# Performance work log

Hardware: AMD Instinct MI355X
Metric: run time of the kernel (lower is better)

The kernel has to match this reference:

```python
import jax, jax.numpy as jnp
import numpy as np

PARENTS = [-1, 0, 0, 0, 1, 2, 3, 4, 5, 6, 7, 8, 9, 9, 9, 12, 13, 14, 16, 17, 18, 19, 20, 21]
K = 24          # num_joints (SMPL kinematic tree)
BONE = 12       # 3x3 rotation (9) + 3 rel offset
FEAT = 64       # local_feature_size
B = 65536       # batch
NIN = BONE + 1 + FEAT  # 77: bone_transform(13) concat parent feature(64)


def setup_inputs() -> dict:
    key = jax.random.key(0)
    ks = jax.random.split(key, 6)
    pose = jax.random.normal(ks[0], (B, K, 3, 3), jnp.float32)
    rel_joints = jax.random.normal(ks[1], (B, K, 3), jnp.float32)
    # proj_bone_prior: Linear(K*BONE -> FEAT)
    Wp = jax.random.normal(ks[2], (K * BONE, FEAT), jnp.float32) * 0.05
    bp = jnp.zeros((FEAT,), jnp.float32)
    # per-joint BoneMLP: Linear(NIN->NIN), ReLU, Linear(NIN->FEAT), ReLU (stacked over K)
    W1 = jax.random.normal(ks[3], (K, NIN, NIN), jnp.float32) * 0.05
    b1 = jnp.zeros((K, NIN), jnp.float32)
    W2 = jax.random.normal(ks[4], (K, NIN, FEAT), jnp.float32) * 0.05
    b2 = jnp.zeros((K, FEAT), jnp.float32)
    return {"pose": pose, "rel_joints": rel_joints, "Wp": Wp, "bp": bp,
            "W1": W1, "b1": b1, "W2": W2, "b2": b2}


def reference(pose, rel_joints, Wp, bp, W1, b1, W2, b2):
    Bn, Kn = rel_joints.shape[0], rel_joints.shape[1]
    bone_lengths = jnp.linalg.norm(rel_joints, axis=-1, keepdims=True)          # B,K,1
    bone_features = jnp.concatenate([pose.reshape(Bn, Kn, 9), rel_joints], -1)  # B,K,12
    root_bone_prior = bone_features.reshape(Bn, -1) @ Wp + bp                   # B,FEAT
    bone_transforms = jnp.concatenate([bone_features, bone_lengths], -1)        # B,K,13
    feats = [None] * Kn
    for i in range(Kn):  # fixed structural loop over kinematic tree (K=24)
        parent = PARENTS[i]
        pf = root_bone_prior if parent == -1 else feats[parent]
        x = jnp.concatenate([bone_transforms[:, i, :], pf], axis=-1)  # B,77
        h = jax.nn.relu(x @ W1[i] + b1[i])
        feats[i] = jax.nn.relu(h @ W2[i] + b2[i])
    return jnp.concatenate(feats, axis=-1)  # B, K*FEAT
```

## Files before the change

### kernel.cpp

```cpp
#include <hip/hip_runtime.h>
#include <hip/hip_bf16.h>
#include <math.h>

typedef __attribute__((ext_vector_type(8))) short short8;
typedef __attribute__((ext_vector_type(4))) short s4;
typedef __attribute__((ext_vector_type(4))) float f32x4;

#define NJ 24

#define F1_J   7680
#define F2_OFF (NJ*F1_J)
#define F2_J   6144
#define FP_OFF (F2_OFF + NJ*F2_J)
#define IMG_SHORTS (FP_OFF + 36*512)

#define MFMA(A,B,C) __builtin_amdgcn_mfma_f32_16x16x32_bf16((A),(B),(C),0,0,0)

__constant__ int ORD[24] = {0,1,4,7,10, 2,5,8,11, 3,6,9, 12,15, 13,16,18,20,22, 14,17,19,21,23};
__constant__ int PSL[24] = {1,0,1,1,1,  0,1,1,1,  0,0,0,  0,1,   0,1,1,1,1,    0,0,0,0,0};
__constant__ int SSL[24] = {0,1,1,1,-1, 1,1,1,-1, 0,0,0,  1,-1,  1,1,1,1,-1,   0,0,0,0,-1};

__device__ __forceinline__ short f2bf(float f) {
  union { float f; unsigned u; } v; v.f = f;
  unsigned r = v.u + 0x7FFFu + ((v.u >> 16) & 1u);
  return (short)(r >> 16);
}
__device__ __forceinline__ short sbf(float f) {
  __hip_bfloat16 h = __float2bfloat16(f);
  return *reinterpret_cast<short*>(&h);
}
__device__ __forceinline__ short8 pk8(f32x4 lo, f32x4 hi) {
  union { short8 s; unsigned u[4]; } r;
  asm("v_cvt_pk_bf16_f32 %0, %1, %2" : "=v"(r.u[0]) : "v"(lo[0]), "v"(lo[1]));
  asm("v_cvt_pk_bf16_f32 %0, %1, %2" : "=v"(r.u[1]) : "v"(lo[2]), "v"(lo[3]));
  asm("v_cvt_pk_bf16_f32 %0, %1, %2" : "=v"(r.u[2]) : "v"(hi[0]), "v"(hi[1]));
  asm("v_cvt_pk_bf16_f32 %0, %1, %2" : "=v"(r.u[3]) : "v"(hi[2]), "v"(hi[3]));
  return r.s;
}
__device__ __forceinline__ s4 pk4(f32x4 v) {
  union { s4 s; unsigned u[2]; } r;
  asm("v_cvt_pk_bf16_f32 %0, %1, %2" : "=v"(r.u[0]) : "v"(v[0]), "v"(v[1]));
  asm("v_cvt_pk_bf16_f32 %0, %1, %2" : "=v"(r.u[1]) : "v"(v[2]), "v"(v[3]));
  return r.s;
}
__device__ __forceinline__ f32x4 relu4(f32x4 v) {
  f32x4 r; r[0]=fmaxf(v[0],0.f); r[1]=fmaxf(v[1],0.f);
  r[2]=fmaxf(v[2],0.f); r[3]=fmaxf(v[3],0.f); return r;
}

__global__ __launch_bounds__(256) void prep_kernel(
    const float* __restrict__ W1, const float* __restrict__ W2,
    const float* __restrict__ Wp, const float* __restrict__ b1,
    const float* __restrict__ b2, short* __restrict__ img) {
  int t = blockIdx.x * 256 + threadIdx.x;
  if (t >= IMG_SHORTS) return;
  float v = 0.f;
  if (t < F2_OFF) {
    int i = t / F1_J, r = t % F1_J;
    int blk = r >> 9, q = r & 511;
    int ln = q >> 3, e = q & 7;
    int nt = blk / 3, s = blk - nt*3;
    int n  = nt*16 + (ln & 15);
    int kp = s*32 + (ln >> 4)*8 + e;
    if (kp == 13) {
      v = (n < 77) ? b1[i*77 + n] : (n == 77 ? 1.f : 0.f);
    } else if (n < 77) {
      if (kp < 13)                  v = W1[i*5929 + kp*77 + n];
      else if (kp >= 16 && kp < 80) v = W1[i*5929 + (kp-3)*77 + n];
    }
  } else if (t < FP_OFF) {
    int u = t - F2_OFF;
    int i = u / F2_J, r = u % F2_J;
    int blk = r >> 9, q = r & 511;
    int ln = q >> 3, e = q & 7;
    int nt = blk / 3, s = blk - nt*3;
    int n  = nt*16 + (ln & 15);
    int k  = s*32 + (ln >> 4)*8 + e;
    if (k < 77)       v = W2[i*4928 + k*64 + n];
    else if (k == 77) v = b2[i*64 + n];
  } else {
    int u = t - FP_OFF;
    int blk = u >> 9, q = u & 511;
    int ln = q >> 3, e = q & 7;
    int nt = blk / 9, s = blk - nt*9;
    int n  = nt*16 + (ln & 15);
    int kp = s*32 + (ln >> 4)*8 + e;
    int j, w;
    if (kp < 216) { j = kp / 9;       w = kp % 9; }
    else          { j = (kp-216) / 3; w = 9 + (kp-216) % 3; }
    v = Wp[(j*12 + w)*64 + n];
  }
  img[t] = f2bf(v);
}

#define ISSUE_W1(JN) do { \
  unsigned long long _b = img_u + (unsigned long long)(JN)*15360ull; \
  asm volatile( \
    "global_load_dwordx4 %0, %15, %16\n"  "global_load_dwordx4 %1, %15, %16 offset:1024\n" \
    "global_load_dwordx4 %2, %15, %16 offset:2048\n" "global_load_dwordx4 %3, %15, %16 offset:3072\n" \
    "global_load_dwordx4 %4, %15, %17\n"  "global_load_dwordx4 %5, %15, %17 offset:1024\n" \
    "global_load_dwordx4 %6, %15, %17 offset:2048\n" "global_load_dwordx4 %7, %15, %17 offset:3072\n" \
    "global_load_dwordx4 %8, %15, %18\n"  "global_load_dwordx4 %9, %15, %18 offset:1024\n" \
    "global_load_dwordx4 %10, %15, %18 offset:2048\n" "global_load_dwordx4 %11, %15, %18 offset:3072\n" \
    "global_load_dwordx4 %12, %15, %19\n" "global_load_dwordx4 %13, %15, %19 offset:1024\n" \
    "global_load_dwordx4 %14, %15, %19 offset:2048\n" \
    : "=&v"(fw1[0]),"=&v"(fw1[1]),"=&v"(fw1[2]),"=&v"(fw1[3]),"=&v"(fw1[4]), \
      "=&v"(fw1[5]),"=&v"(fw1[6]),"=&v"(fw1[7]),"=&v"(fw1[8]),"=&v"(fw1[9]), \
      "=&v"(fw1[10]),"=&v"(fw1[11]),"=&v"(fw1[12]),"=&v"(fw1[13]),"=&v"(fw1[14]) \
    : "v"(voff), "s"(_b), "s"(_b+4096ull), "s"(_b+8192ull), "s"(_b+12288ull) \
    : "memory"); \
} while(0)

#define ISSUE_BTW2(J) do { \
  unsigned long long _b = img_u + 368640ull + (unsigned long long)(J)*12288ull; \
  asm volatile( \
    "global_load_dwordx4 %12, %26, %27\n" "global_load_dwordx4 %13, %26, %27 offset:1024\n" \
    "global_load_dwordx4 %14, %26, %27 offset:2048\n" "global_load_dwordx4 %15, %26, %27 offset:3072\n" \
    "global_load_dwordx4 %16, %26, %28\n" "global_load_dwordx4 %17, %26, %28 offset:1024\n" \
    "global_load_dwordx4 %18, %26, %28 offset:2048\n" "global_load_dwordx4 %19, %26, %28 offset:3072\n" \
    "global_load_dwordx4 %20, %26, %29\n" "global_load_dwordx4 %21, %26, %29 offset:1024\n" \
    "global_load_dwordx4 %22, %26, %29 offset:2048\n" "global_load_dwordx4 %23, %26, %29 offset:3072\n" \
    "global_load_dword %0, %24, off\n" \
    "global_load_dword %1, %24, off offset:4\n" \
    "global_load_dword %2, %24, off offset:8\n" \
    "global_load_dword %3, %24, off offset:12\n" \
    "global_load_dword %4, %24, off offset:16\n" \
    "global_load_dword %5, %24, off offset:20\n" \
    "global_load_dword %6, %24, off offset:24\n" \
    "global_load_dword %7, %24, off offset:28\n" \
    "global_load_dword %8, %24, off offset:32\n" \
    "global_load_dword %9, %25, off\n" \
    "global_load_dword %10, %25, off offset:4\n" \
    "global_load_dword %11, %25, off offset:8\n" \
    : "=&v"(d0),"=&v"(d1),"=&v"(d2),"=&v"(d3),"=&v"(d4),"=&v"(d5), \
      "=&v"(d6),"=&v"(d7),"=&v"(d8),"=&v"(d9),"=&v"(d10),"=&v"(d11), \
      "=&v"(fw2[0]),"=&v"(fw2[1]),"=&v"(fw2[2]),"=&v"(fw2[3]),"=&v"(fw2[4]),"=&v"(fw2[5]), \
      "=&v"(fw2[6]),"=&v"(fw2[7]),"=&v"(fw2[8]),"=&v"(fw2[9]),"=&v"(fw2[10]),"=&v"(fw2[11]) \
    : "v"(aP), "v"(aR), "v"(voff), \
      "s"(_b), "s"(_b+4096ull), "s"(_b+8192ull) \
    : "memory"); \
} while(0)

#define WAITV(N) do { asm volatile("s_waitcnt vmcnt(" #N ")" ::: "memory"); \
                      __builtin_amdgcn_sched_barrier(0); } while(0)

__global__ __launch_bounds__(256, 1) void enc_kernel(
    const float* __restrict__ pose, const float* __restrict__ rel,
    const float* __restrict__ bp,  const short* __restrict__ img,
    float* __restrict__ out) {
  __shared__ __align__(16) short lds[4*15360];

  const int tid  = threadIdx.x;
  const int lane = tid & 63;
  const int wv   = tid >> 6;
  short* myl   = lds + wv*15360;
  short* featL = myl;
  short* hL    = myl + 9216;
  short* btL   = myl + 14336;

  const int cl  = lane & 15;
  const int g   = lane >> 4;
  const int rw0 = blockIdx.x*256 + wv*64;
  const short8 zz = {0,0,0,0,0,0,0,0};
  const unsigned long long img_u  = (unsigned long long)img;
  const unsigned long long pose_u = (unsigned long long)pose;
  const unsigned long long rel_u  = (unsigned long long)rel;
  const unsigned voff = (unsigned)lane << 4;
  const unsigned long long btP = pose_u + (unsigned long long)(rw0 + lane)*864ull;
  const unsigned long long btR = rel_u  + (unsigned long long)(rw0 + lane)*288ull;

  short8 fw1[15], fw2[12];
  float d0,d1,d2,d3,d4,d5,d6,d7,d8,d9,d10,d11;

  {
    const float* pb = pose + (size_t)(rw0 + lane)*216;
    const float* rb = rel  + (size_t)(rw0 + lane)*72;
    float p0=pb[0],p1=pb[1],p2=pb[2],p3=pb[3],p4=pb[4],p5=pb[5],p6=pb[6],p7=pb[7],p8=pb[8];
    float r0=rb[0],r1=rb[1],r2=rb[2];
    float nv = sqrtf(r0*r0 + r1*r1 + r2*r2);
    short8 wlo = pk8((f32x4){p0,p1,p2,p3}, (f32x4){p4,p5,p6,p7});
    short8 whi;
    whi[0]=sbf(p8); whi[1]=sbf(r0); whi[2]=sbf(r1); whi[3]=sbf(r2);
    whi[4]=sbf(nv); whi[5]=(short)0x3F80; whi[6]=0; whi[7]=0;
    *(short8*)(btL + lane*16)     = wlo;
    *(short8*)(btL + lane*16 + 8) = whi;
  }

#pragma unroll 1
  for (int m = 0; m < 4; ++m) {
    const float* pr = pose + (size_t)(rw0 + m*16 + cl)*216;
    const float* rr = rel  + (size_t)(rw0 + m*16 + cl)*72;
    const short8* fpg = (const short8*)(img + FP_OFF) + lane;
    short8 av[9];
#pragma unroll
    for (int s = 0; s < 9; ++s) {
      int k0 = s*32 + g*8;
      const float* sp = (k0 < 216) ? (pr + k0) : (rr + (k0 - 216));
      av[s] = pk8(*(const f32x4*)sp, *(const f32x4*)(sp + 4));
    }
#pragma unroll
    for (int nt = 0; nt < 4; ++nt) {
      f32x4 c = {0,0,0,0};
#pragma unroll
      for (int s = 0; s < 9; ++s) c = MFMA(fpg[(nt*9 + s)*64], av[s], c);
      f32x4 bb = *(const f32x4*)(bp + nt*16 + g*4);
      c[0]+=bb[0]; c[1]+=bb[1]; c[2]+=bb[2]; c[3]+=bb[3];
      *(s4*)(featL + 4608 + (m*16 + cl)*72 + nt*16 + g*4) = pk4(c);
    }
  }

  ISSUE_W1(0);

#pragma unroll 1
  for (int p = 0; p < NJ; ++p) {
    const int j  = ORD[p];
    const int ps = PSL[p];
    const int ss = SSL[p];
    const int jn = (p < NJ-1) ? ORD[p+1] : 0;

    const unsigned long long aP = btP + (unsigned long long)(jn*36);
    const unsigned long long aR = btR + (unsigned long long)(jn*12);
    ISSUE_BTW2(j);

    WAITV(24);

#pragma unroll
    for (int m = 0; m < 4; ++m) {
      const short* fb = featL + ps*4608 + (m*16 + cl)*72;
      short8 a0 = (g < 2) ? *(const short8*)(btL + (m*16 + cl)*16 + g*8)
                          : *(const short8*)(fb + (g-2)*8);
      short8 a1 = *(const short8*)(fb + 16 + g*8);
      short8 a2 = (g < 2) ? *(const short8*)(fb + 48 + g*8) : zz;
#pragma unroll
      for (int nt = 0; nt < 5; ++nt) {
        f32x4 c = {0,0,0,0};
        c = MFMA(fw1[nt*3+0], a0, c);
        c = MFMA(fw1[nt*3+1], a1, c);
        c = MFMA(fw1[nt*3+2], a2, c);
        *(s4*)(hL + (m*16 + cl)*80 + nt*16 + g*4) = pk4(relu4(c));
      }
    }

    WAITV(0);

    {
      float nv = sqrtf(d9*d9 + d10*d10 + d11*d11);
      short8 wlo = pk8((f32x4){d0,d1,d2,d3}, (f32x4){d4,d5,d6,d7});
      short8 whi;
      whi[0]=sbf(d8); whi[1]=sbf(d9); whi[2]=sbf(d10); whi[3]=sbf(d11);
      whi[4]=sbf(nv); whi[5]=(short)0x3F80; whi[6]=0; whi[7]=0;
      *(short8*)(btL + lane*16)     = wlo;
      *(short8*)(btL + lane*16 + 8) = whi;
    }

#pragma unroll
    for (int m = 0; m < 4; ++m) {
      const short* hb = hL + (m*16 + cl)*80;
      short8 h0 = *(const short8*)(hb + g*8);
      short8 h1 = *(const short8*)(hb + 32 + g*8);
      short8 h2 = (g < 2) ? *(const short8*)(hb + 64 + g*8) : zz;
#pragma unroll
      for (int nt = 0; nt < 4; ++nt) {
        f32x4 c = {0,0,0,0};
        c = MFMA(fw2[nt*3+0], h0, c);
        c = MFMA(fw2[nt*3+1], h1, c);
        c = MFMA(fw2[nt*3+2], h2, c);
        f32x4 v = relu4(c);
        float* o = out + (size_t)(rw0 + m*16 + cl)*1536 + (size_t)j*64 + nt*16 + g*4;
        __builtin_nontemporal_store(v, (f32x4*)o);
        if (ss >= 0)
          *(s4*)(featL + ss*4608 + (m*16 + cl)*72 + nt*16 + g*4) = pk4(v);
      }
    }

    ISSUE_W1(jn);
  }
}

extern "C" void kernel_launch(void* const* d_in, const int* in_sizes, int n_in,
                              void* d_out, int out_size, void* d_ws, size_t ws_size,
                              hipStream_t stream) {
  const float* pose = (const float*)d_in[0];
  const float* rel  = (const float*)d_in[1];
  const float* Wp   = (const float*)d_in[2];
  const float* bp   = (const float*)d_in[3];
  const float* W1   = (const float*)d_in[4];
  const float* b1   = (const float*)d_in[5];
  const float* W2   = (const float*)d_in[6];
  const float* b2   = (const float*)d_in[7];
  float* outp = (float*)d_out;
  short* img  = (short*)d_ws;
  const int Bn = in_sizes[0] / 216;
  prep_kernel<<<(IMG_SHORTS + 255)/256, 256, 0, stream>>>(W1, W2, Wp, b1, b2, img);
  enc_kernel<<<Bn/256, 256, 0, stream>>>(pose, rel, bp, img, outp);
}
```

Measured before the change: 149.0 us.

## Double-buffer per-joint weight registers and prefetch next joint's W1, W2 and bone inputs

Splits the weight fragments into two register sets (a/b). Each joint's body now issues the next joint's W1, W2 and bone-transform loads in the middle of the current joint, between the two MLP layers, so their latency overlaps the layer-2 MFMAs and stores. Before, W2 and the bone loads were issued at the start of the same iteration that used them. The loop is manually unrolled by two to alternate buffers, and the separate prologue bone load is folded into the first prefetch. This roughly doubles weight-register usage and relies on vmcnt counting to cover the non-temporal stores.

```diff
diff --git a/kernel.cpp b/kernel.cpp
--- a/kernel.cpp
+++ b/kernel.cpp
@@ -93,7 +93,7 @@
   img[t] = f2bf(v);
 }
 
-#define ISSUE_W1(JN) do { \
+#define ISSUE_W1_INTO(ARR, JN) do { \
   unsigned long long _b = img_u + (unsigned long long)(JN)*15360ull; \
   asm volatile( \
     "global_load_dwordx4 %0, %15, %16\n"  "global_load_dwordx4 %1, %15, %16 offset:1024\n" \
@@ -104,14 +104,14 @@
     "global_load_dwordx4 %10, %15, %18 offset:2048\n" "global_load_dwordx4 %11, %15, %18 offset:3072\n" \
     "global_load_dwordx4 %12, %15, %19\n" "global_load_dwordx4 %13, %15, %19 offset:1024\n" \
     "global_load_dwordx4 %14, %15, %19 offset:2048\n" \
-    : "=&v"(fw1[0]),"=&v"(fw1[1]),"=&v"(fw1[2]),"=&v"(fw1[3]),"=&v"(fw1[4]), \
-      "=&v"(fw1[5]),"=&v"(fw1[6]),"=&v"(fw1[7]),"=&v"(fw1[8]),"=&v"(fw1[9]), \
-      "=&v"(fw1[10]),"=&v"(fw1[11]),"=&v"(fw1[12]),"=&v"(fw1[13]),"=&v"(fw1[14]) \
+    : "=&v"(ARR[0]),"=&v"(ARR[1]),"=&v"(ARR[2]),"=&v"(ARR[3]),"=&v"(ARR[4]), \
+      "=&v"(ARR[5]),"=&v"(ARR[6]),"=&v"(ARR[7]),"=&v"(ARR[8]),"=&v"(ARR[9]), \
+      "=&v"(ARR[10]),"=&v"(ARR[11]),"=&v"(ARR[12]),"=&v"(ARR[13]),"=&v"(ARR[14]) \
     : "v"(voff), "s"(_b), "s"(_b+4096ull), "s"(_b+8192ull), "s"(_b+12288ull) \
     : "memory"); \
 } while(0)
 
-#define ISSUE_BTW2(J) do { \
+#define ISSUE_BTW2_INTO(W2A, J) do { \
   unsigned long long _b = img_u + 368640ull + (unsigned long long)(J)*12288ull; \
   asm volatile( \
     "global_load_dwordx4 %12, %26, %27\n" "global_load_dwordx4 %13, %26, %27 offset:1024\n" \
@@ -134,8 +134,8 @@
     "global_load_dword %11, %25, off offset:8\n" \
     : "=&v"(d0),"=&v"(d1),"=&v"(d2),"=&v"(d3),"=&v"(d4),"=&v"(d5), \
       "=&v"(d6),"=&v"(d7),"=&v"(d8),"=&v"(d9),"=&v"(d10),"=&v"(d11), \
-      "=&v"(fw2[0]),"=&v"(fw2[1]),"=&v"(fw2[2]),"=&v"(fw2[3]),"=&v"(fw2[4]),"=&v"(fw2[5]), \
-      "=&v"(fw2[6]),"=&v"(fw2[7]),"=&v"(fw2[8]),"=&v"(fw2[9]),"=&v"(fw2[10]),"=&v"(fw2[11]) \
+      "=&v"(W2A[0]),"=&v"(W2A[1]),"=&v"(W2A[2]),"=&v"(W2A[3]),"=&v"(W2A[4]),"=&v"(W2A[5]), \
+      "=&v"(W2A[6]),"=&v"(W2A[7]),"=&v"(W2A[8]),"=&v"(W2A[9]),"=&v"(W2A[10]),"=&v"(W2A[11]) \
     : "v"(aP), "v"(aR), "v"(voff), \
       "s"(_b), "s"(_b+4096ull), "s"(_b+8192ull) \
     : "memory"); \
@@ -143,6 +143,68 @@
 
 #define WAITV(N) do { asm volatile("s_waitcnt vmcnt(" #N ")" ::: "memory"); \
                       __builtin_amdgcn_sched_barrier(0); } while(0)
+
+#define BODY(P, F1C, F2C, F1N, F2N, CW) do { \
+    const int j  = ORD[P]; \
+    const int ps = PSL[P]; \
+    const int ss = SSL[P]; \
+    const int jn = ((P)+1 < NJ) ? ORD[(P)+1] : 0; \
+    WAITV(CW); \
+     \
+    { \
+      float nv = sqrtf(d9*d9 + d10*d10 + d11*d11); \
+      short8 wlo = pk8((f32x4){d0,d1,d2,d3}, (f32x4){d4,d5,d6,d7}); \
+      short8 whi; \
+      whi[0]=sbf(d8); whi[1]=sbf(d9); whi[2]=sbf(d10); whi[3]=sbf(d11); \
+      whi[4]=sbf(nv); whi[5]=(short)0x3F80; whi[6]=0; whi[7]=0; \
+      *(short8*)(btL + lane*16)     = wlo; \
+      *(short8*)(btL + lane*16 + 8) = whi; \
+    } \
+     \
+    _Pragma("unroll") \
+    for (int m = 0; m < 4; ++m) { \
+      const short* fb = featL + ps*4608 + (m*16 + cl)*72; \
+      short8 a0 = (g < 2) ? *(const short8*)(btL + (m*16 + cl)*16 + g*8) \
+                          : *(const short8*)(fb + (g-2)*8); \
+      short8 a1 = *(const short8*)(fb + 16 + g*8); \
+      short8 a2 = (g < 2) ? *(const short8*)(fb + 48 + g*8) : zz; \
+      _Pragma("unroll") \
+      for (int nt = 0; nt < 5; ++nt) { \
+        f32x4 c = {0,0,0,0}; \
+        c = MFMA(F1C[nt*3+0], a0, c); \
+        c = MFMA(F1C[nt*3+1], a1, c); \
+        c = MFMA(F1C[nt*3+2], a2, c); \
+        *(s4*)(hL + (m*16 + cl)*80 + nt*16 + g*4) = pk4(relu4(c)); \
+      } \
+    } \
+     \
+    { \
+      const unsigned long long aP = btP + (unsigned long long)(jn*36); \
+      const unsigned long long aR = btR + (unsigned long long)(jn*12); \
+      ISSUE_W1_INTO(F1N, jn); \
+      ISSUE_BTW2_INTO(F2N, jn); \
+    } \
+     \
+    _Pragma("unroll") \
+    for (int m = 0; m < 4; ++m) { \
+      const short* hb = hL + (m*16 + cl)*80; \
+      short8 h0 = *(const short8*)(hb + g*8); \
+      short8 h1 = *(const short8*)(hb + 32 + g*8); \
+      short8 h2 = (g < 2) ? *(const short8*)(hb + 64 + g*8) : zz; \
+      _Pragma("unroll") \
+      for (int nt = 0; nt < 4; ++nt) { \
+        f32x4 c = {0,0,0,0}; \
+        c = MFMA(F2C[nt*3+0], h0, c); \
+        c = MFMA(F2C[nt*3+1], h1, c); \
+        c = MFMA(F2C[nt*3+2], h2, c); \
+        f32x4 v = relu4(c); \
+        float* o = out + (size_t)(rw0 + m*16 + cl)*1536 + (size_t)j*64 + nt*16 + g*4; \
+        __builtin_nontemporal_store(v, (f32x4*)o); \
+        if (ss >= 0) \
+          *(s4*)(featL + ss*4608 + (m*16 + cl)*72 + nt*16 + g*4) = pk4(v); \
+      } \
+    } \
+  } while(0)
 
 __global__ __launch_bounds__(256, 1) void enc_kernel(
     const float* __restrict__ pose, const float* __restrict__ rel,
@@ -169,22 +231,8 @@
   const unsigned long long btP = pose_u + (unsigned long long)(rw0 + lane)*864ull;
   const unsigned long long btR = rel_u  + (unsigned long long)(rw0 + lane)*288ull;
 
-  short8 fw1[15], fw2[12];
+  short8 fw1a[15], fw2a[12], fw1b[15], fw2b[12];
   float d0,d1,d2,d3,d4,d5,d6,d7,d8,d9,d10,d11;
-
-  {
-    const float* pb = pose + (size_t)(rw0 + lane)*216;
-    const float* rb = rel  + (size_t)(rw0 + lane)*72;
-    float p0=pb[0],p1=pb[1],p2=pb[2],p3=pb[3],p4=pb[4],p5=pb[5],p6=pb[6],p7=pb[7],p8=pb[8];
-    float r0=rb[0],r1=rb[1],r2=rb[2];
-    float nv = sqrtf(r0*r0 + r1*r1 + r2*r2);
-    short8 wlo = pk8((f32x4){p0,p1,p2,p3}, (f32x4){p4,p5,p6,p7});
-    short8 whi;
-    whi[0]=sbf(p8); whi[1]=sbf(r0); whi[2]=sbf(r1); whi[3]=sbf(r2);
-    whi[4]=sbf(nv); whi[5]=(short)0x3F80; whi[6]=0; whi[7]=0;
-    *(short8*)(btL + lane*16)     = wlo;
-    *(short8*)(btL + lane*16 + 8) = whi;
-  }
 
 #pragma unroll 1
   for (int m = 0; m < 4; ++m) {
@@ -209,71 +257,20 @@
     }
   }
 
-  ISSUE_W1(0);
-
+  {
+    const unsigned long long aP = btP;
+    const unsigned long long aR = btR;
+    ISSUE_W1_INTO(fw1a, 0);
+    ISSUE_BTW2_INTO(fw2a, 0);
+  }
+
+  BODY(0, fw1a, fw2a, fw1b, fw2b, 0);
+  BODY(1, fw1b, fw2b, fw1a, fw2a, 16);
 #pragma unroll 1
-  for (int p = 0; p < NJ; ++p) {
-    const int j  = ORD[p];
-    const int ps = PSL[p];
-    const int ss = SSL[p];
-    const int jn = (p < NJ-1) ? ORD[p+1] : 0;
-
-    const unsigned long long aP = btP + (unsigned long long)(jn*36);
-    const unsigned long long aR = btR + (unsigned long long)(jn*12);
-    ISSUE_BTW2(j);
-
-    WAITV(24);
-
-#pragma unroll
-    for (int m = 0; m < 4; ++m) {
-      const short* fb = featL + ps*4608 + (m*16 + cl)*72;
-      short8 a0 = (g < 2) ? *(const short8*)(btL + (m*16 + cl)*16 + g*8)
-                          : *(const short8*)(fb + (g-2)*8);
-      short8 a1 = *(const short8*)(fb + 16 + g*8);
-      short8 a2 = (g < 2) ? *(const short8*)(fb + 48 + g*8) : zz;
-#pragma unroll
-      for (int nt = 0; nt < 5; ++nt) {
-        f32x4 c = {0,0,0,0};
-        c = MFMA(fw1[nt*3+0], a0, c);
-        c = MFMA(fw1[nt*3+1], a1, c);
-        c = MFMA(fw1[nt*3+2], a2, c);
-        *(s4*)(hL + (m*16 + cl)*80 + nt*16 + g*4) = pk4(relu4(c));
-      }
-    }
-
-    WAITV(0);
-
-    {
-      float nv = sqrtf(d9*d9 + d10*d10 + d11*d11);
-      short8 wlo = pk8((f32x4){d0,d1,d2,d3}, (f32x4){d4,d5,d6,d7});
-      short8 whi;
-      whi[0]=sbf(d8); whi[1]=sbf(d9); whi[2]=sbf(d10); whi[3]=sbf(d11);
-      whi[4]=sbf(nv); whi[5]=(short)0x3F80; whi[6]=0; whi[7]=0;
-      *(short8*)(btL + lane*16)     = wlo;
-      *(short8*)(btL + lane*16 + 8) = whi;
-    }
-
-#pragma unroll
-    for (int m = 0; m < 4; ++m) {
-      const short* hb = hL + (m*16 + cl)*80;
-      short8 h0 = *(const short8*)(hb + g*8);
-      short8 h1 = *(const short8*)(hb + 32 + g*8);
-      short8 h2 = (g < 2) ? *(const short8*)(hb + 64 + g*8) : zz;
-#pragma unroll
-      for (int nt = 0; nt < 4; ++nt) {
-        f32x4 c = {0,0,0,0};
-        c = MFMA(fw2[nt*3+0], h0, c);
-        c = MFMA(fw2[nt*3+1], h1, c);
-        c = MFMA(fw2[nt*3+2], h2, c);
-        f32x4 v = relu4(c);
-        float* o = out + (size_t)(rw0 + m*16 + cl)*1536 + (size_t)j*64 + nt*16 + g*4;
-        __builtin_nontemporal_store(v, (f32x4*)o);
-        if (ss >= 0)
-          *(s4*)(featL + ss*4608 + (m*16 + cl)*72 + nt*16 + g*4) = pk4(v);
-      }
-    }
-
-    ISSUE_W1(jn);
+  for (int q = 1; q < 12; ++q) {
+    const int p = 2*q;
+    BODY(p,     fw1a, fw2a, fw1b, fw2b, 16);
+    BODY(p + 1, fw1b, fw2b, fw1a, fw2a, 16);
   }
 }
 
```

Result: slower. 189.2 us (+27.0%).
